# Kernel tuning notes

Hardware: AMD Instinct MI355X
Metric: run time of the kernel (lower is better)

## Reference

```python
import jax, jax.numpy as jnp
import numpy as np

LN_EPS = 1e-5
MODEL_DIM = 256
HEADS = 4


def layer_norm(x, gamma, beta):
    mu = jnp.mean(x, axis=-1, keepdims=True)
    var = jnp.var(x, axis=-1, keepdims=True)
    return (x - mu) * jax.lax.rsqrt(var + LN_EPS) * gamma + beta


def setup_inputs() -> dict:
    key = jax.random.key(0)
    ks = jax.random.split(key, 4)
    bs, s, d, h = 4, 2048, MODEL_DIM, HEADS
    x = jax.random.normal(ks[0], (bs, s, d), dtype=jnp.float32)
    Wq = jax.random.normal(ks[1], (d, h * d), dtype=jnp.float32) / np.sqrt(d)
    Wk = jax.random.normal(ks[2], (d, h * d), dtype=jnp.float32) / np.sqrt(d)
    Wv = jax.random.normal(ks[3], (h * d, d), dtype=jnp.float32) / np.sqrt(h * d)
    gamma = jnp.ones((d,), dtype=jnp.float32)
    beta = jnp.zeros((d,), dtype=jnp.float32)
    return {"x": x, "Wq": Wq, "Wk": Wk, "Wv": Wv, "gamma": gamma, "beta": beta}


def reference(x, Wq, Wk, Wv, gamma, beta):
    bs, s, d = x.shape
    h = Wq.shape[1] // d
    sqrt_norm = jnp.float32(np.sqrt(d))
    # pre_norm = False -> no input LN
    # NOTE: torch does .view(bs, h, s, d) on the (bs, s, h*d) projection --
    # a raw C-order reinterpretation, reproduced here by jnp.reshape.
    Q = jnp.reshape(x @ Wq, (bs, h, s, d))
    K = jnp.reshape(x @ Wk, (bs, h, s, d))
    scores = jnp.einsum('bhid,bhjd->bhij', Q, K)
    probs = jax.nn.softmax(scores / sqrt_norm, axis=-1)  # (bs, h, s, s)
    # value is the shared raw input x broadcast across heads
    out = jnp.einsum('bhij,bjd->bhid', probs, x)
    out = jnp.transpose(out, (0, 2, 1, 3)).reshape(bs, s, h * d)
    out = out @ Wv + x
    out = layer_norm(out, gamma, beta)  # post-norm
    return out, probs
```

## Files before the change

kernel.cpp:

```cpp
#include <hip/hip_runtime.h>

typedef __bf16 bf16;
typedef __bf16 bf16x4 __attribute__((ext_vector_type(4)));
typedef __bf16 bf16x8 __attribute__((ext_vector_type(8)));
typedef float f32x4 __attribute__((ext_vector_type(4)));

#define BS 4
#define S 2048
#define D 256
#define H 4
#define HD 1024
#define NROW 8192

__device__ __forceinline__ void load_lds16(const bf16* g, bf16* l) {
    __builtin_amdgcn_global_load_lds(
        (const __attribute__((address_space(1))) void*)g,
        (__attribute__((address_space(3))) void*)l, 16, 0, 0);
}

__global__ __launch_bounds__(256) void prep_x(const float* __restrict__ x,
                                              bf16* __restrict__ x_bf,
                                              bf16* __restrict__ xT_bf) {
    __shared__ bf16 tile[64][68];
    int j0 = blockIdx.x * 64, d0 = blockIdx.y * 64, b = blockIdx.z;
    int t = threadIdx.x;
    int rsub = t >> 4;
    int c4 = (t & 15) * 4;
#pragma unroll
    for (int rr = 0; rr < 4; rr++) {
        int j = rr * 16 + rsub;
        float4 v = *(const float4*)&x[((size_t)(b * S + j0 + j)) * D + d0 + c4];
        bf16 b0 = (bf16)v.x, b1 = (bf16)v.y, b2 = (bf16)v.z, b3 = (bf16)v.w;
        tile[j][c4 + 0] = b0;
        tile[j][c4 + 1] = b1;
        tile[j][c4 + 2] = b2;
        tile[j][c4 + 3] = b3;
        bf16x4 o = {b0, b1, b2, b3};
        *(bf16x4*)&x_bf[((size_t)(b * S + j0 + j)) * D + d0 + c4] = o;
    }
    __syncthreads();
#pragma unroll
    for (int rr = 0; rr < 4; rr++) {
        int dd = rr * 16 + rsub;
        bf16x4 o;
        o[0] = tile[c4 + 0][dd];
        o[1] = tile[c4 + 1][dd];
        o[2] = tile[c4 + 2][dd];
        o[3] = tile[c4 + 3][dd];
        *(bf16x4*)&xT_bf[(size_t)b * D * S + (size_t)(d0 + dd) * S + j0 + c4] = o;
    }
}

__device__ __forceinline__ void tile_tr64(const float* __restrict__ src,
                                          bf16* __restrict__ dst, int ldsrc,
                                          int lddst, int r0, int c0, float scale,
                                          bf16 (&tile)[64][68], int t) {
    int rsub = t >> 4, c4 = (t & 15) * 4;
#pragma unroll
    for (int rr = 0; rr < 4; rr++) {
        int r = rr * 16 + rsub;
        float4 v = *(const float4*)&src[(size_t)(r0 + r) * ldsrc + c0 + c4];
        tile[r][c4 + 0] = (bf16)(v.x * scale);
        tile[r][c4 + 1] = (bf16)(v.y * scale);
        tile[r][c4 + 2] = (bf16)(v.z * scale);
        tile[r][c4 + 3] = (bf16)(v.w * scale);
    }
    __syncthreads();
#pragma unroll
    for (int rr = 0; rr < 4; rr++) {
        int c = rr * 16 + rsub;
        bf16x4 o;
        o[0] = tile[c4 + 0][c];
        o[1] = tile[c4 + 1][c];
        o[2] = tile[c4 + 2][c];
        o[3] = tile[c4 + 3][c];
        *(bf16x4*)&dst[(size_t)(c0 + c) * lddst + r0 + c4] = o;
    }
}

__global__ __launch_bounds__(256) void prep_w(const float* __restrict__ Wq,
                                              const float* __restrict__ Wk,
                                              const float* __restrict__ Wv,
                                              bf16* __restrict__ WqT,
                                              bf16* __restrict__ WkT,
                                              bf16* __restrict__ WvT) {
    __shared__ bf16 tile[64][68];
    const float SCALE = 0.09016844005556021f;
    int bx = blockIdx.x, t = threadIdx.x;
    if (bx < 64) {
        int rt = bx & 3, ct = bx >> 2;
        tile_tr64(Wq, WqT, HD, D, rt * 64, ct * 64, SCALE, tile, t);
    } else if (bx < 128) {
        int b2 = bx - 64;
        int rt = b2 & 3, ct = b2 >> 2;
        tile_tr64(Wk, WkT, HD, D, rt * 64, ct * 64, 1.0f, tile, t);
    } else {
        int b2 = bx - 128;
        int rt = b2 & 15, ct = b2 >> 4;
        tile_tr64(Wv, WvT, D, HD, rt * 64, ct * 64, 1.0f, tile, t);
    }
}

__global__ __launch_bounds__(256) void gemm_nt_bf16(
    const bf16* __restrict__ A, const bf16* __restrict__ B0,
    const bf16* __restrict__ B1, bf16* __restrict__ C0, bf16* __restrict__ C1,
    int N, int Kd) {
    const bf16* B = blockIdx.z ? B1 : B0;
    bf16* C = blockIdx.z ? C1 : C0;
    int n0 = blockIdx.x * 64;
    int m0 = blockIdx.y * 64;
    __shared__ __align__(16) bf16 As[64 * 256];
    __shared__ __align__(16) bf16 Bs[64 * 256];
    int t = threadIdx.x, w = t >> 6, l = t & 63;
    int lr = l & 15, lq = l >> 4;
#pragma unroll
    for (int n = 0; n < 8; n++) {
        int r = w * 16 + 2 * n + (l >> 5);
        int cg = (l & 31) ^ (r & 7);
        load_lds16(&A[(size_t)(m0 + r) * D + cg * 8], &As[(w * 16 + 2 * n) * 256]);
        load_lds16(&B[(size_t)(n0 + r) * D + cg * 8], &Bs[(w * 16 + 2 * n) * 256]);
    }
    asm volatile("s_waitcnt vmcnt(0)" ::: "memory");
    __builtin_amdgcn_s_barrier();
    f32x4 acc[4] = {};
#pragma unroll
    for (int kf = 0; kf < 8; kf++) {
        bf16x8 af = *(const bf16x8*)&As[(w * 16 + lr) * 256 + (((kf * 4 + lq) ^ (lr & 7)) * 8)];
#pragma unroll
        for (int nt = 0; nt < 4; nt++) {
            bf16x8 bfr =
                *(const bf16x8*)&Bs[(nt * 16 + lr) * 256 + (((kf * 4 + lq) ^ (lr & 7)) * 8)];
            acc[nt] = __builtin_amdgcn_mfma_f32_16x16x32_bf16(af, bfr, acc[nt], 0, 0, 0);
        }
    }
#pragma unroll
    for (int nt = 0; nt < 4; nt++)
#pragma unroll
        for (int rr = 0; rr < 4; rr++) {
            int row = m0 + w * 16 + lq * 4 + rr;
            C[(size_t)row * N + n0 + nt * 16 + lr] = (bf16)acc[nt][rr];
        }
}

__device__ __forceinline__ void stage_k_tile(const bf16* __restrict__ K,
                                             bf16* kb, int j0, int w, int l) {
    int krow = (w << 3) + (l >> 5);
    int kc = l & 31;
#pragma unroll
    for (int n = 0; n < 4; n++) {
        int r = krow + (n << 1);
        int cg = kc ^ (r & 7);
        load_lds16(&K[(size_t)(j0 + r) * D + cg * 8], &kb[((w << 3) + (n << 1)) * 256]);
    }
}

__device__ __forceinline__ void stage_x_tile(const bf16* __restrict__ xTb,
                                             bf16* xb, int j0, int w, int l) {
    int xrow = (w << 6) + (l >> 2);
    int xc = l & 3;
#pragma unroll
    for (int n = 0; n < 4; n++) {
        int dd = xrow + (n << 4);
        int cg = xc ^ ((dd >> 1) & 3);
        load_lds16(&xTb[(size_t)dd * S + j0 + cg * 8], &xb[((w << 6) + (n << 4)) * 32]);
    }
}

__global__ __launch_bounds__(256, 2) void attn_fused(
    const bf16* __restrict__ Qbf, const bf16* __restrict__ Kbf,
    const bf16* __restrict__ xT, float* __restrict__ probs,
    bf16* __restrict__ attn) {
    int nblk = blockIdx.x;
    int lb = (nblk & 7) * 64 + (nblk >> 3);
    int bh = lb >> 5, b = bh >> 2, h = bh & 3;
    int t = threadIdx.x, w = t >> 6, l = t & 63;
    int lr = l & 15, lq = l >> 4;
    const bf16* Q = Qbf + (size_t)bh * S * D;
    const bf16* K = Kbf + (size_t)bh * S * D;
    const bf16* xTb = xT + (size_t)b * D * S;
    int ibase = (lb & 31) * 64 + w * 16;

    __shared__ __align__(16) bf16 kbuf[2][32 * 256];
    __shared__ __align__(16) bf16 xbuf[2][256 * 32];
    __shared__ __align__(16) bf16 pl[4][16 * 40];

    bf16x8 qf[8];
#pragma unroll
    for (int kf = 0; kf < 8; kf++)
        qf[kf] = *(const bf16x8*)&Q[(size_t)(ibase + lr) * D + kf * 32 + lq * 8];

    float lsum[4] = {0.f, 0.f, 0.f, 0.f};
    stage_k_tile(K, kbuf[0], 0, w, l);
    for (int it = 0; it < 64; it++) {
        int cur = it & 1;
        if (it < 63) {
            stage_k_tile(K, kbuf[cur ^ 1], (it + 1) << 5, w, l);
            asm volatile("s_waitcnt vmcnt(4)" ::: "memory");
        } else {
            asm volatile("s_waitcnt vmcnt(0)" ::: "memory");
        }
        __builtin_amdgcn_s_barrier();
#pragma unroll
        for (int subj = 0; subj < 2; subj++) {
            f32x4 acc = {};
#pragma unroll
            for (int kf = 0; kf < 8; kf++) {
                bf16x8 kfr = *(const bf16x8*)
                    &kbuf[cur][(subj * 16 + lr) * 256 + (((kf * 4 + lq) ^ (lr & 7)) * 8)];
                acc = __builtin_amdgcn_mfma_f32_16x16x32_bf16(qf[kf], kfr, acc, 0, 0, 0);
            }
#pragma unroll
            for (int r = 0; r < 4; r++) lsum[r] += exp2f(acc[r]);
        }
        __builtin_amdgcn_s_barrier();
    }
    float li[4];
#pragma unroll
    for (int r = 0; r < 4; r++) {
        float s = lsum[r];
        for (int off = 1; off < 16; off <<= 1) s += __shfl_xor(s, off);
        li[r] = 1.0f / s;
    }

    f32x4 oacc[16] = {};
    float* probb = probs + (size_t)bh * S * S;
    stage_k_tile(K, kbuf[0], 0, w, l);
    stage_x_tile(xTb, xbuf[0], 0, w, l);
    for (int it = 0; it < 64; it++) {
        int cur = it & 1;
        int j0 = it << 5;
        if (it < 63) {
            stage_k_tile(K, kbuf[cur ^ 1], j0 + 32, w, l);
            stage_x_tile(xTb, xbuf[cur ^ 1], j0 + 32, w, l);
            asm volatile("s_waitcnt vmcnt(8)" ::: "memory");
        } else {
            asm volatile("s_waitcnt vmcnt(0)" ::: "memory");
        }
        __builtin_amdgcn_s_barrier();
#pragma unroll
        for (int subj = 0; subj < 2; subj++) {
            f32x4 acc = {};
#pragma unroll
            for (int kf = 0; kf < 8; kf++) {
                bf16x8 kfr = *(const bf16x8*)
                    &kbuf[cur][(subj * 16 + lr) * 256 + (((kf * 4 + lq) ^ (lr & 7)) * 8)];
                acc = __builtin_amdgcn_mfma_f32_16x16x32_bf16(qf[kf], kfr, acc, 0, 0, 0);
            }
#pragma unroll
            for (int r = 0; r < 4; r++) {
                float p = exp2f(acc[r]) * li[r];
                pl[w][(lq * 4 + r) * 40 + subj * 16 + lr] = (bf16)p;
            }
        }
        bf16x8 pf = *(const bf16x8*)&pl[w][lr * 40 + lq * 8];
        f32x4 p0, p1;
#pragma unroll
        for (int e = 0; e < 4; e++) { p0[e] = (float)pf[e]; p1[e] = (float)pf[e + 4]; }
        float* pp = &probb[(size_t)(ibase + lr) * S + j0 + lq * 8];
        *(f32x4*)pp = p0;
        *(f32x4*)(pp + 4) = p1;
#pragma unroll
        for (int dt = 0; dt < 16; dt++) {
            int dd = dt * 16 + lr;
            bf16x8 xf =
                *(const bf16x8*)&xbuf[cur][dd * 32 + ((lq ^ ((lr >> 1) & 3)) * 8)];
            oacc[dt] = __builtin_amdgcn_mfma_f32_16x16x32_bf16(pf, xf, oacc[dt], 0, 0, 0);
        }
        __builtin_amdgcn_s_barrier();
    }
#pragma unroll
    for (int dt = 0; dt < 16; dt++)
#pragma unroll
        for (int rr = 0; rr < 4; rr++) {
            int row = ibase + lq * 4 + rr;
            attn[((size_t)(b * S + row)) * HD + h * D + dt * 16 + lr] = (bf16)oacc[dt][rr];
        }
}

__global__ __launch_bounds__(256) void out_gemm_ln(
    const bf16* __restrict__ attn, const bf16* __restrict__ WvT,
    const float* __restrict__ x, const float* __restrict__ gamma,
    const float* __restrict__ beta, float* __restrict__ out) {
    int m0 = blockIdx.x * 16;
    int t = threadIdx.x, w = t >> 6, l = t & 63;
    int lr = l & 15, lq = l >> 4;
    int ncol0 = w * 64;
    f32x4 acc[4] = {};
    for (int k0 = 0; k0 < HD; k0 += 32) {
        bf16x8 af = *(const bf16x8*)&attn[(size_t)(m0 + lr) * HD + k0 + lq * 8];
#pragma unroll
        for (int dt = 0; dt < 4; dt++) {
            bf16x8 bfr =
                *(const bf16x8*)&WvT[(size_t)(ncol0 + dt * 16 + lr) * HD + k0 + lq * 8];
            acc[dt] = __builtin_amdgcn_mfma_f32_16x16x32_bf16(af, bfr, acc[dt], 0, 0, 0);
        }
    }
    float sum[4] = {0, 0, 0, 0}, sq[4] = {0, 0, 0, 0};
#pragma unroll
    for (int dt = 0; dt < 4; dt++)
#pragma unroll
        for (int rr = 0; rr < 4; rr++) {
            int row = m0 + lq * 4 + rr;
            float v = acc[dt][rr] + x[(size_t)row * D + ncol0 + dt * 16 + lr];
            acc[dt][rr] = v;
            sum[rr] += v;
            sq[rr] += v * v;
        }
#pragma unroll
    for (int rr = 0; rr < 4; rr++)
        for (int off = 1; off < 16; off <<= 1) {
            sum[rr] += __shfl_xor(sum[rr], off);
            sq[rr] += __shfl_xor(sq[rr], off);
        }
    __shared__ float part[4][16][2];
    if (lr == 0)
#pragma unroll
        for (int rr = 0; rr < 4; rr++) {
            part[w][lq * 4 + rr][0] = sum[rr];
            part[w][lq * 4 + rr][1] = sq[rr];
        }
    __syncthreads();
    float mu[4], rs[4];
#pragma unroll
    for (int rr = 0; rr < 4; rr++) {
        int rowi = lq * 4 + rr;
        float s = part[0][rowi][0] + part[1][rowi][0] + part[2][rowi][0] + part[3][rowi][0];
        float q = part[0][rowi][1] + part[1][rowi][1] + part[2][rowi][1] + part[3][rowi][1];
        mu[rr] = s * (1.0f / 256.0f);
        float var = q * (1.0f / 256.0f) - mu[rr] * mu[rr];
        rs[rr] = rsqrtf(var + 1e-5f);
    }
#pragma unroll
    for (int dt = 0; dt < 4; dt++) {
        int col = ncol0 + dt * 16 + lr;
        float g = gamma[col], be = beta[col];
#pragma unroll
        for (int rr = 0; rr < 4; rr++) {
            float v = (acc[dt][rr] - mu[rr]) * rs[rr] * g + be;
            out[(size_t)(m0 + lq * 4 + rr) * D + col] = v;
        }
    }
}

extern "C" void kernel_launch(void* const* d_in, const int* in_sizes, int n_in,
                              void* d_out, int out_size, void* d_ws, size_t ws_size,
                              hipStream_t stream) {
    const float* x = (const float*)d_in[0];
    const float* Wq = (const float*)d_in[1];
    const float* Wk = (const float*)d_in[2];
    const float* Wv = (const float*)d_in[3];
    const float* gamma = (const float*)d_in[4];
    const float* beta = (const float*)d_in[5];
    float* out = (float*)d_out;
    float* probs = out + (size_t)NROW * D;

    char* ws = (char*)d_ws;
    bf16* x_bf = (bf16*)ws;
    bf16* xT_bf = (bf16*)(ws + 4194304);
    bf16* WqT = (bf16*)(ws + 8388608);
    bf16* WkT = (bf16*)(ws + 8912896);
    bf16* WvT = (bf16*)(ws + 9437184);
    bf16* Qbf = (bf16*)(ws + 9961472);
    bf16* Kbf = (bf16*)(ws + 26738688);
    bf16* attn = (bf16*)(ws + 43515904);

    prep_x<<<dim3(32, 4, 4), 256, 0, stream>>>(x, x_bf, xT_bf);
    prep_w<<<192, 256, 0, stream>>>(Wq, Wk, Wv, WqT, WkT, WvT);
    gemm_nt_bf16<<<dim3(16, 128, 2), 256, 0, stream>>>(x_bf, WqT, WkT, Qbf, Kbf,
                                                       HD, D);
    attn_fused<<<dim3(512), 256, 0, stream>>>(Qbf, Kbf, xT_bf, probs, attn);
    out_gemm_ln<<<512, 256, 0, stream>>>(attn, WvT, x, gamma, beta, out);
}
```

Before: 490.4 us.

## Split key range across two wave groups and give each wave 32 query rows

The attention kernel now runs 512-thread blocks with two groups of four waves. Each group handles alternating 32-key tiles, and each wave processes two 16-row query tiles so every K and x fragment loaded from LDS feeds two MFMAs. Row sums and output accumulators are combined across the groups through shared memory. The aim is to cut LDS traffic per MFMA and halve the number of blocks. In exchange it doubles accumulator registers, which risks spills under the 512-thread, two-block launch bound. It also uses nearly all of LDS, limiting occupancy to one block per CU.

```diff
diff --git a/kernel.cpp b/kernel.cpp
--- a/kernel.cpp
+++ b/kernel.cpp
@@ -143,138 +143,199 @@
 }
 
 __device__ __forceinline__ void stage_k_tile(const bf16* __restrict__ K,
-                                             bf16* kb, int j0, int w, int l) {
-    int krow = (w << 3) + (l >> 5);
+                                             bf16* kb, int j0, int lw, int l) {
+    int krow = (lw << 3) + (l >> 5);
     int kc = l & 31;
 #pragma unroll
     for (int n = 0; n < 4; n++) {
         int r = krow + (n << 1);
         int cg = kc ^ (r & 7);
-        load_lds16(&K[(size_t)(j0 + r) * D + cg * 8], &kb[((w << 3) + (n << 1)) * 256]);
+        load_lds16(&K[(size_t)(j0 + r) * D + cg * 8], &kb[((lw << 3) + (n << 1)) * 256]);
     }
 }
 
 __device__ __forceinline__ void stage_x_tile(const bf16* __restrict__ xTb,
-                                             bf16* xb, int j0, int w, int l) {
-    int xrow = (w << 6) + (l >> 2);
+                                             bf16* xb, int j0, int lw, int l) {
+    int xrow = (lw << 6) + (l >> 2);
     int xc = l & 3;
 #pragma unroll
     for (int n = 0; n < 4; n++) {
         int dd = xrow + (n << 4);
         int cg = xc ^ ((dd >> 1) & 3);
-        load_lds16(&xTb[(size_t)dd * S + j0 + cg * 8], &xb[((w << 6) + (n << 4)) * 32]);
-    }
-}
-
-__global__ __launch_bounds__(256, 2) void attn_fused(
+        load_lds16(&xTb[(size_t)dd * S + j0 + cg * 8], &xb[((lw << 6) + (n << 4)) * 32]);
+    }
+}
+
+__global__ __launch_bounds__(512, 2) void attn_fused(
     const bf16* __restrict__ Qbf, const bf16* __restrict__ Kbf,
     const bf16* __restrict__ xT, float* __restrict__ probs,
     bf16* __restrict__ attn) {
     int nblk = blockIdx.x;
-    int lb = (nblk & 7) * 64 + (nblk >> 3);
-    int bh = lb >> 5, b = bh >> 2, h = bh & 3;
+    int lb = (nblk & 7) * 32 + (nblk >> 3);
+    int bh = lb >> 4, b = bh >> 2, h = bh & 3;
+    int strip = lb & 15;
     int t = threadIdx.x, w = t >> 6, l = t & 63;
+    int lw = w & 3, g = w >> 2;
     int lr = l & 15, lq = l >> 4;
     const bf16* Q = Qbf + (size_t)bh * S * D;
     const bf16* K = Kbf + (size_t)bh * S * D;
     const bf16* xTb = xT + (size_t)b * D * S;
-    int ibase = (lb & 31) * 64 + w * 16;
-
-    __shared__ __align__(16) bf16 kbuf[2][32 * 256];
-    __shared__ __align__(16) bf16 xbuf[2][256 * 32];
-    __shared__ __align__(16) bf16 pl[4][16 * 40];
-
-    bf16x8 qf[8];
-#pragma unroll
-    for (int kf = 0; kf < 8; kf++)
-        qf[kf] = *(const bf16x8*)&Q[(size_t)(ibase + lr) * D + kf * 32 + lq * 8];
-
-    float lsum[4] = {0.f, 0.f, 0.f, 0.f};
-    stage_k_tile(K, kbuf[0], 0, w, l);
-    for (int it = 0; it < 64; it++) {
+    int ibase = strip * 128 + lw * 32;
+
+    __shared__ __align__(16) char smem[151552];
+    bf16* kbg = (bf16*)smem + (size_t)g * 2 * 8192;
+    bf16* xbg = (bf16*)(smem + 65536) + (size_t)g * 2 * 8192;
+    bf16* plw = (bf16*)(smem + 131072) + w * (32 * 40);
+
+    bf16x8 qf[2][8];
+#pragma unroll
+    for (int hi = 0; hi < 2; hi++)
+#pragma unroll
+        for (int kf = 0; kf < 8; kf++)
+            qf[hi][kf] = *(const bf16x8*)
+                &Q[(size_t)(ibase + hi * 16 + lr) * D + kf * 32 + lq * 8];
+
+    float lsum[2][4] = {};
+    stage_k_tile(K, kbg, g << 5, lw, l);
+    for (int it = 0; it < 32; it++) {
         int cur = it & 1;
-        if (it < 63) {
-            stage_k_tile(K, kbuf[cur ^ 1], (it + 1) << 5, w, l);
+        if (it < 31) {
+            stage_k_tile(K, kbg + (cur ^ 1) * 8192, (2 * (it + 1) + g) << 5, lw, l);
             asm volatile("s_waitcnt vmcnt(4)" ::: "memory");
         } else {
             asm volatile("s_waitcnt vmcnt(0)" ::: "memory");
         }
         __builtin_amdgcn_s_barrier();
+        const bf16* kbc = kbg + cur * 8192;
 #pragma unroll
         for (int subj = 0; subj < 2; subj++) {
-            f32x4 acc = {};
+            f32x4 a0 = {}, a1 = {};
 #pragma unroll
             for (int kf = 0; kf < 8; kf++) {
                 bf16x8 kfr = *(const bf16x8*)
-                    &kbuf[cur][(subj * 16 + lr) * 256 + (((kf * 4 + lq) ^ (lr & 7)) * 8)];
-                acc = __builtin_amdgcn_mfma_f32_16x16x32_bf16(qf[kf], kfr, acc, 0, 0, 0);
-            }
-#pragma unroll
-            for (int r = 0; r < 4; r++) lsum[r] += exp2f(acc[r]);
+                    &kbc[(subj * 16 + lr) * 256 + (((kf * 4 + lq) ^ (lr & 7)) * 8)];
+                a0 = __builtin_amdgcn_mfma_f32_16x16x32_bf16(qf[0][kf], kfr, a0, 0, 0, 0);
+                a1 = __builtin_amdgcn_mfma_f32_16x16x32_bf16(qf[1][kf], kfr, a1, 0, 0, 0);
+            }
+#pragma unroll
+            for (int r = 0; r < 4; r++) {
+                lsum[0][r] += exp2f(a0[r]);
+                lsum[1][r] += exp2f(a1[r]);
+            }
         }
         __builtin_amdgcn_s_barrier();
     }
-    float li[4];
-#pragma unroll
-    for (int r = 0; r < 4; r++) {
-        float s = lsum[r];
-        for (int off = 1; off < 16; off <<= 1) s += __shfl_xor(s, off);
-        li[r] = 1.0f / s;
-    }
-
-    f32x4 oacc[16] = {};
+#pragma unroll
+    for (int hi = 0; hi < 2; hi++)
+#pragma unroll
+        for (int r = 0; r < 4; r++) {
+            float s = lsum[hi][r];
+            for (int off = 1; off < 16; off <<= 1) s += __shfl_xor(s, off);
+            lsum[hi][r] = s;
+        }
+    {
+        float* lex = (float*)smem;
+        f32x4 v0 = {lsum[0][0], lsum[0][1], lsum[0][2], lsum[0][3]};
+        f32x4 v1 = {lsum[1][0], lsum[1][1], lsum[1][2], lsum[1][3]};
+        *(f32x4*)&lex[(w * 64 + l) * 8] = v0;
+        *(f32x4*)&lex[(w * 64 + l) * 8 + 4] = v1;
+        __syncthreads();
+        f32x4 o0 = *(const f32x4*)&lex[((w ^ 4) * 64 + l) * 8];
+        f32x4 o1 = *(const f32x4*)&lex[((w ^ 4) * 64 + l) * 8 + 4];
+#pragma unroll
+        for (int r = 0; r < 4; r++) {
+            lsum[0][r] = 1.0f / (lsum[0][r] + o0[r]);
+            lsum[1][r] = 1.0f / (lsum[1][r] + o1[r]);
+        }
+        __syncthreads();
+    }
+
+    f32x4 oacc0[16] = {};
+    f32x4 oacc1[16] = {};
     float* probb = probs + (size_t)bh * S * S;
-    stage_k_tile(K, kbuf[0], 0, w, l);
-    stage_x_tile(xTb, xbuf[0], 0, w, l);
-    for (int it = 0; it < 64; it++) {
+    stage_k_tile(K, kbg, g << 5, lw, l);
+    stage_x_tile(xTb, xbg, g << 5, lw, l);
+    for (int it = 0; it < 32; it++) {
         int cur = it & 1;
-        int j0 = it << 5;
-        if (it < 63) {
-            stage_k_tile(K, kbuf[cur ^ 1], j0 + 32, w, l);
-            stage_x_tile(xTb, xbuf[cur ^ 1], j0 + 32, w, l);
+        int j0 = (2 * it + g) << 5;
+        if (it < 31) {
+            int jn = (2 * (it + 1) + g) << 5;
+            stage_k_tile(K, kbg + (cur ^ 1) * 8192, jn, lw, l);
+            stage_x_tile(xTb, xbg + (cur ^ 1) * 8192, jn, lw, l);
             asm volatile("s_waitcnt vmcnt(8)" ::: "memory");
         } else {
             asm volatile("s_waitcnt vmcnt(0)" ::: "memory");
         }
         __builtin_amdgcn_s_barrier();
+        const bf16* kbc = kbg + cur * 8192;
+        const bf16* xbc = xbg + cur * 8192;
 #pragma unroll
         for (int subj = 0; subj < 2; subj++) {
-            f32x4 acc = {};
+            f32x4 a0 = {}, a1 = {};
 #pragma unroll
             for (int kf = 0; kf < 8; kf++) {
                 bf16x8 kfr = *(const bf16x8*)
-                    &kbuf[cur][(subj * 16 + lr) * 256 + (((kf * 4 + lq) ^ (lr & 7)) * 8)];
-                acc = __builtin_amdgcn_mfma_f32_16x16x32_bf16(qf[kf], kfr, acc, 0, 0, 0);
+                    &kbc[(subj * 16 + lr) * 256 + (((kf * 4 + lq) ^ (lr & 7)) * 8)];
+                a0 = __builtin_amdgcn_mfma_f32_16x16x32_bf16(qf[0][kf], kfr, a0, 0, 0, 0);
+                a1 = __builtin_amdgcn_mfma_f32_16x16x32_bf16(qf[1][kf], kfr, a1, 0, 0, 0);
             }
 #pragma unroll
             for (int r = 0; r < 4; r++) {
-                float p = exp2f(acc[r]) * li[r];
-                pl[w][(lq * 4 + r) * 40 + subj * 16 + lr] = (bf16)p;
-            }
-        }
-        bf16x8 pf = *(const bf16x8*)&pl[w][lr * 40 + lq * 8];
-        f32x4 p0, p1;
-#pragma unroll
-        for (int e = 0; e < 4; e++) { p0[e] = (float)pf[e]; p1[e] = (float)pf[e + 4]; }
-        float* pp = &probb[(size_t)(ibase + lr) * S + j0 + lq * 8];
-        *(f32x4*)pp = p0;
-        *(f32x4*)(pp + 4) = p1;
+                float p0 = exp2f(a0[r]) * lsum[0][r];
+                float p1 = exp2f(a1[r]) * lsum[1][r];
+                plw[(lq * 4 + r) * 40 + subj * 16 + lr] = (bf16)p0;
+                plw[(16 + lq * 4 + r) * 40 + subj * 16 + lr] = (bf16)p1;
+            }
+        }
+        bf16x8 pf0 = *(const bf16x8*)&plw[lr * 40 + lq * 8];
+        bf16x8 pf1 = *(const bf16x8*)&plw[(16 + lr) * 40 + lq * 8];
+        {
+            f32x4 s0, s1;
+#pragma unroll
+            for (int e = 0; e < 4; e++) { s0[e] = (float)pf0[e]; s1[e] = (float)pf0[e + 4]; }
+            float* pp = &probb[(size_t)(ibase + lr) * S + j0 + lq * 8];
+            *(f32x4*)pp = s0;
+            *(f32x4*)(pp + 4) = s1;
+#pragma unroll
+            for (int e = 0; e < 4; e++) { s0[e] = (float)pf1[e]; s1[e] = (float)pf1[e + 4]; }
+            float* pq = &probb[(size_t)(ibase + 16 + lr) * S + j0 + lq * 8];
+            *(f32x4*)pq = s0;
+            *(f32x4*)(pq + 4) = s1;
+        }
 #pragma unroll
         for (int dt = 0; dt < 16; dt++) {
             int dd = dt * 16 + lr;
-            bf16x8 xf =
-                *(const bf16x8*)&xbuf[cur][dd * 32 + ((lq ^ ((lr >> 1) & 3)) * 8)];
-            oacc[dt] = __builtin_amdgcn_mfma_f32_16x16x32_bf16(pf, xf, oacc[dt], 0, 0, 0);
+            bf16x8 xf = *(const bf16x8*)&xbc[dd * 32 + ((lq ^ ((lr >> 1) & 3)) * 8)];
+            oacc0[dt] = __builtin_amdgcn_mfma_f32_16x16x32_bf16(pf0, xf, oacc0[dt], 0, 0, 0);
+            oacc1[dt] = __builtin_amdgcn_mfma_f32_16x16x32_bf16(pf1, xf, oacc1[dt], 0, 0, 0);
         }
         __builtin_amdgcn_s_barrier();
     }
-#pragma unroll
-    for (int dt = 0; dt < 16; dt++)
-#pragma unroll
-        for (int rr = 0; rr < 4; rr++) {
-            int row = ibase + lq * 4 + rr;
-            attn[((size_t)(b * S + row)) * HD + h * D + dt * 16 + lr] = (bf16)oacc[dt][rr];
-        }
+
+    float* osh = (float*)smem;
+    if (g == 1) {
+#pragma unroll
+        for (int dt = 0; dt < 16; dt++)
+#pragma unroll
+            for (int rr = 0; rr < 4; rr++) {
+                osh[(lw * 32 + lq * 4 + rr) * 258 + dt * 16 + lr] = oacc0[dt][rr];
+                osh[(lw * 32 + 16 + lq * 4 + rr) * 258 + dt * 16 + lr] = oacc1[dt][rr];
+            }
+    }
+    __syncthreads();
+    if (g == 0) {
+#pragma unroll
+        for (int dt = 0; dt < 16; dt++)
+#pragma unroll
+            for (int rr = 0; rr < 4; rr++) {
+                float v0 = oacc0[dt][rr] + osh[(lw * 32 + lq * 4 + rr) * 258 + dt * 16 + lr];
+                float v1 = oacc1[dt][rr] + osh[(lw * 32 + 16 + lq * 4 + rr) * 258 + dt * 16 + lr];
+                int r0 = ibase + lq * 4 + rr;
+                int r1 = ibase + 16 + lq * 4 + rr;
+                attn[((size_t)(b * S + r0)) * HD + h * D + dt * 16 + lr] = (bf16)v0;
+                attn[((size_t)(b * S + r1)) * HD + h * D + dt * 16 + lr] = (bf16)v1;
+            }
+    }
 }
 
 __global__ __launch_bounds__(256) void out_gemm_ln(
@@ -368,6 +429,6 @@
     prep_w<<<192, 256, 0, stream>>>(Wq, Wk, Wv, WqT, WkT, WvT);
     gemm_nt_bf16<<<dim3(16, 128, 2), 256, 0, stream>>>(x_bf, WqT, WkT, Qbf, Kbf,
                                                        HD, D);
-    attn_fused<<<dim3(512), 256, 0, stream>>>(Qbf, Kbf, xT_bf, probs, attn);
+    attn_fused<<<dim3(256), 512, 0, stream>>>(Qbf, Kbf, xT_bf, probs, attn);
     out_gemm_ln<<<512, 256, 0, stream>>>(attn, WvT, x, gamma, beta, out);
 }
```

Result: faster. 470.7 us (-4.0%).

## Restructure attention PV loop into ping-pong phases with setprio and remap GEMM block order

Applied to the files above, without the earlier changes.

The second attention pass is split into four phases, each loading LDS fragments into registers, then doing a barrier-separated MFMA burst at raised wave priority. Global prefetch of the next K and x tiles is spread across the phases. Probabilities are now stored in fp32 directly, before bf16 rounding, with a 16-wide store pattern instead of 8-wide vectors. The projection GEMM also gets a remapped block index so that neighbouring blocks land on the same XCD, aiming for better L2 reuse. The extra barriers and the narrower probs stores may add overhead.

```diff
diff --git a/kernel.cpp b/kernel.cpp
--- a/kernel.cpp
+++ b/kernel.cpp
@@ -105,10 +105,13 @@
     const bf16* __restrict__ A, const bf16* __restrict__ B0,
     const bf16* __restrict__ B1, bf16* __restrict__ C0, bf16* __restrict__ C1,
     int N, int Kd) {
-    const bf16* B = blockIdx.z ? B1 : B0;
-    bf16* C = blockIdx.z ? C1 : C0;
-    int n0 = blockIdx.x * 64;
-    int m0 = blockIdx.y * 64;
+    int fid = blockIdx.x + 16 * blockIdx.y + 2048 * blockIdx.z;
+    int lb = (fid & 7) * 512 + (fid >> 3);
+    int z = lb >> 11;
+    const bf16* B = z ? B1 : B0;
+    bf16* C = z ? C1 : C0;
+    int n0 = (lb & 15) * 64;
+    int m0 = ((lb >> 4) & 127) * 64;
     __shared__ __align__(16) bf16 As[64 * 256];
     __shared__ __align__(16) bf16 Bs[64 * 256];
     int t = threadIdx.x, w = t >> 6, l = t & 63;
@@ -203,12 +206,14 @@
 #pragma unroll
         for (int subj = 0; subj < 2; subj++) {
             f32x4 acc = {};
+            __builtin_amdgcn_s_setprio(1);
 #pragma unroll
             for (int kf = 0; kf < 8; kf++) {
                 bf16x8 kfr = *(const bf16x8*)
                     &kbuf[cur][(subj * 16 + lr) * 256 + (((kf * 4 + lq) ^ (lr & 7)) * 8)];
                 acc = __builtin_amdgcn_mfma_f32_16x16x32_bf16(qf[kf], kfr, acc, 0, 0, 0);
             }
+            __builtin_amdgcn_s_setprio(0);
 #pragma unroll
             for (int r = 0; r < 4; r++) lsum[r] += exp2f(acc[r]);
         }
@@ -226,45 +231,81 @@
     float* probb = probs + (size_t)bh * S * S;
     stage_k_tile(K, kbuf[0], 0, w, l);
     stage_x_tile(xTb, xbuf[0], 0, w, l);
+    asm volatile("s_waitcnt vmcnt(0)" ::: "memory");
+    __builtin_amdgcn_s_barrier();
     for (int it = 0; it < 64; it++) {
         int cur = it & 1;
         int j0 = it << 5;
+        const bf16* kbc = kbuf[cur];
+        const bf16* xbc = xbuf[cur];
+
+        if (it < 63) stage_k_tile(K, kbuf[cur ^ 1], j0 + 32, w, l);
+        bf16x8 kf0[8];
+#pragma unroll
+        for (int kf = 0; kf < 8; kf++)
+            kf0[kf] = *(const bf16x8*)&kbc[lr * 256 + (((kf * 4 + lq) ^ (lr & 7)) * 8)];
+        __builtin_amdgcn_s_barrier();
+        f32x4 a0 = {};
+        __builtin_amdgcn_s_setprio(1);
+#pragma unroll
+        for (int kf = 0; kf < 8; kf++)
+            a0 = __builtin_amdgcn_mfma_f32_16x16x32_bf16(qf[kf], kf0[kf], a0, 0, 0, 0);
+        __builtin_amdgcn_s_setprio(0);
+        __builtin_amdgcn_s_barrier();
+
+        if (it < 63) stage_x_tile(xTb, xbuf[cur ^ 1], j0 + 32, w, l);
+        bf16x8 kf1[8];
+#pragma unroll
+        for (int kf = 0; kf < 8; kf++)
+            kf1[kf] = *(const bf16x8*)&kbc[(16 + lr) * 256 + (((kf * 4 + lq) ^ (lr & 7)) * 8)];
+#pragma unroll
+        for (int r = 0; r < 4; r++) {
+            float p = exp2f(a0[r]) * li[r];
+            probb[(size_t)(ibase + lq * 4 + r) * S + j0 + lr] = p;
+            pl[w][(lq * 4 + r) * 40 + lr] = (bf16)p;
+        }
+        __builtin_amdgcn_s_barrier();
+        f32x4 a1 = {};
+        __builtin_amdgcn_s_setprio(1);
+#pragma unroll
+        for (int kf = 0; kf < 8; kf++)
+            a1 = __builtin_amdgcn_mfma_f32_16x16x32_bf16(qf[kf], kf1[kf], a1, 0, 0, 0);
+        __builtin_amdgcn_s_setprio(0);
+        __builtin_amdgcn_s_barrier();
+
+#pragma unroll
+        for (int r = 0; r < 4; r++) {
+            float p = exp2f(a1[r]) * li[r];
+            probb[(size_t)(ibase + lq * 4 + r) * S + j0 + 16 + lr] = p;
+            pl[w][(lq * 4 + r) * 40 + 16 + lr] = (bf16)p;
+        }
+        bf16x8 pf = *(const bf16x8*)&pl[w][lr * 40 + lq * 8];
+        bf16x8 xf0[8];
+#pragma unroll
+        for (int dt = 0; dt < 8; dt++)
+            xf0[dt] = *(const bf16x8*)&xbc[(dt * 16 + lr) * 32 + ((lq ^ ((lr >> 1) & 3)) * 8)];
+        __builtin_amdgcn_s_barrier();
+        __builtin_amdgcn_s_setprio(1);
+#pragma unroll
+        for (int dt = 0; dt < 8; dt++)
+            oacc[dt] = __builtin_amdgcn_mfma_f32_16x16x32_bf16(pf, xf0[dt], oacc[dt], 0, 0, 0);
+        __builtin_amdgcn_s_setprio(0);
+        __builtin_amdgcn_s_barrier();
+
+        bf16x8 xf1[8];
+#pragma unroll
+        for (int dt = 0; dt < 8; dt++)
+            xf1[dt] = *(const bf16x8*)&xbc[((dt + 8) * 16 + lr) * 32 + ((lq ^ ((lr >> 1) & 3)) * 8)];
+        __builtin_amdgcn_s_barrier();
+        __builtin_amdgcn_s_setprio(1);
+#pragma unroll
+        for (int dt = 0; dt < 8; dt++)
+            oacc[dt + 8] = __builtin_amdgcn_mfma_f32_16x16x32_bf16(pf, xf1[dt], oacc[dt + 8], 0, 0, 0);
+        __builtin_amdgcn_s_setprio(0);
         if (it < 63) {
-            stage_k_tile(K, kbuf[cur ^ 1], j0 + 32, w, l);
-            stage_x_tile(xTb, xbuf[cur ^ 1], j0 + 32, w, l);
             asm volatile("s_waitcnt vmcnt(8)" ::: "memory");
         } else {
             asm volatile("s_waitcnt vmcnt(0)" ::: "memory");
-        }
-        __builtin_amdgcn_s_barrier();
-#pragma unroll
-        for (int subj = 0; subj < 2; subj++) {
-            f32x4 acc = {};
-#pragma unroll
-            for (int kf = 0; kf < 8; kf++) {
-                bf16x8 kfr = *(const bf16x8*)
-                    &kbuf[cur][(subj * 16 + lr) * 256 + (((kf * 4 + lq) ^ (lr & 7)) * 8)];
-                acc = __builtin_amdgcn_mfma_f32_16x16x32_bf16(qf[kf], kfr, acc, 0, 0, 0);
-            }
-#pragma unroll
-            for (int r = 0; r < 4; r++) {
-                float p = exp2f(acc[r]) * li[r];
-                pl[w][(lq * 4 + r) * 40 + subj * 16 + lr] = (bf16)p;
-            }
-        }
-        bf16x8 pf = *(const bf16x8*)&pl[w][lr * 40 + lq * 8];
-        f32x4 p0, p1;
-#pragma unroll
-        for (int e = 0; e < 4; e++) { p0[e] = (float)pf[e]; p1[e] = (float)pf[e + 4]; }
-        float* pp = &probb[(size_t)(ibase + lr) * S + j0 + lq * 8];
-        *(f32x4*)pp = p0;
-        *(f32x4*)(pp + 4) = p1;
-#pragma unroll
-        for (int dt = 0; dt < 16; dt++) {
-            int dd = dt * 16 + lr;
-            bf16x8 xf =
-                *(const bf16x8*)&xbuf[cur][dd * 32 + ((lq ^ ((lr >> 1) & 3)) * 8)];
-            oacc[dt] = __builtin_amdgcn_mfma_f32_16x16x32_bf16(pf, xf, oacc[dt], 0, 0, 0);
         }
         __builtin_amdgcn_s_barrier();
     }
```

After: 493.0 us. About the same (+0.5%).
